# Kernel tuning notes

Hardware: AMD Instinct MI355X
Metric: run time of the kernel (lower is better)

The kernel has to match this reference:

```python
import jax, jax.numpy as jnp
import numpy as np

B, L, F, H, DIM = 32, 1024, 1024, 1024, 1024


def setup_inputs() -> dict:
    key = jax.random.key(0)
    ks = jax.random.split(key, 8)
    features = jax.random.normal(ks[0], (B, L, F), dtype=jnp.float32)
    hidden = jax.random.normal(ks[1], (B, H), dtype=jnp.float32)
    # Dense layer params (glorot-ish scale)
    W1 = jax.random.normal(ks[2], (F, DIM), dtype=jnp.float32) / np.sqrt(F)
    b1 = jnp.zeros((DIM,), dtype=jnp.float32)
    W2 = jax.random.normal(ks[3], (H, DIM), dtype=jnp.float32) / np.sqrt(H)
    b2 = jnp.zeros((DIM,), dtype=jnp.float32)
    Wp = jax.random.normal(ks[4], (DIM, 1), dtype=jnp.float32) / np.sqrt(DIM)
    bp = jnp.zeros((1,), dtype=jnp.float32)
    return {"features": features, "hidden": hidden, "W1": W1, "b1": b1,
            "W2": W2, "b2": b2, "Wp": Wp, "bp": bp}


def reference(features, hidden, W1, b1, W2, b2, Wp, bp):
    # features: [B, L, F], hidden: [B, H]
    h1 = jnp.einsum('blf,fd->bld', features, W1) + b1          # [B, L, D]
    h2 = (hidden @ W2 + b2)[:, None, :]                         # [B, 1, D]
    att = jnp.tanh(h1 + h2)                                     # [B, L, D]
    score = jnp.einsum('bld,do->blo', att, Wp) + bp             # [B, L, 1]
    attention_weights = jax.nn.softmax(score, axis=1)           # [B, L, 1]
    context_vector = jnp.sum(attention_weights * features, axis=1)  # [B, F]
    return context_vector
```

## Files before the change

kernel.cpp:

```cpp
#include <hip/hip_runtime.h>
#include <hip/hip_bf16.h>


typedef __attribute__((ext_vector_type(8))) __bf16 bf16x8;
typedef __attribute__((ext_vector_type(4))) float f32x4;

static __device__ __forceinline__ ushort f2bf(float x) {
  unsigned u = __float_as_uint(x);
  return (ushort)((u + 0x7fffu + ((u >> 16) & 1u)) >> 16);
}

static __device__ __forceinline__ int2 cvt4(float4 v) {
  __hip_bfloat162 c0 = __float22bfloat162_rn({v.x, v.y});
  __hip_bfloat162 c1 = __float22bfloat162_rn({v.z, v.w});
  int2 r;
  r.x = *(int*)&c0;
  r.y = *(int*)&c1;
  return r;
}

static __device__ __forceinline__ float tanh_fast(float x) {
  float e = __expf(2.f * x);
  return 1.f - 2.f / (e + 1.f);
}

__global__ __launch_bounds__(256) void prep_kernel(
    const float* __restrict__ W1, ushort* __restrict__ w1t,
    const float* __restrict__ hidden, const float* __restrict__ W2,
    const float* __restrict__ b2, float* __restrict__ h2p) {
  __shared__ float smem[64 * 65];
  const int bx = blockIdx.x, tid = threadIdx.x;
  if (bx < 256) {
    const int tc = bx & 15, tr = bx >> 4;
    float (*tt)[65] = (float(*)[65])smem;
    const int r = tid >> 4, c4 = (tid & 15) * 4;
#pragma unroll
    for (int p = 0; p < 4; ++p) {
      const int rr = p * 16 + r;
      float4 v = *(const float4*)(W1 + (size_t)(tr * 64 + rr) * 1024 + tc * 64 + c4);
      tt[rr][c4] = v.x; tt[rr][c4 + 1] = v.y; tt[rr][c4 + 2] = v.z; tt[rr][c4 + 3] = v.w;
    }
    __syncthreads();
    const int cc = tid >> 3, r8 = (tid & 7) * 8;
#pragma unroll
    for (int p = 0; p < 2; ++p) {
      const int c = p * 32 + cc;
      ushort tmp[8];
#pragma unroll
      for (int j = 0; j < 8; ++j) tmp[j] = f2bf(tt[r8 + j][c]);
      *(int4*)(w1t + (size_t)(tc * 64 + c) * 1024 + tr * 64 + r8) = *(int4*)tmp;
    }
  } else {
    const int t = bx - 256;
    const int dblk = t & 3, b = (t >> 2) & 31, z = t >> 7;
    const int d = dblk * 256 + tid;
    const int k0 = z * 128;
    float* h = smem;
    if (tid < 128) h[tid] = hidden[b * 1024 + k0 + tid];
    __syncthreads();
    float acc = (z == 0) ? b2[d] : 0.f;
#pragma unroll 8
    for (int k = 0; k < 128; ++k)
      acc += h[k] * W2[(size_t)(k0 + k) * 1024 + d];
    h2p[z * 32768 + b * 1024 + d] = acc;
  }
}


__global__ __launch_bounds__(512, 2) void gemm_score_kernel(
    const float* __restrict__ feat,
    const ushort* __restrict__ w1t,
    const float* __restrict__ b1, const float* __restrict__ h2p,
    const float* __restrict__ wp, float* __restrict__ score) {
  __shared__ ushort ldsA[2][64][32];
  __shared__ float hbl[1024], wpl[1024];
  __shared__ float sred[7][64];

  const int tid = threadIdx.x;
  const int row0 = blockIdx.x * 64;
  const int b = blockIdx.x >> 4;
  const int wave = tid >> 6, lane = tid & 63;
  const int lrow = lane & 15, quad = lane >> 4;

  {
    const int d = tid * 2;
    float2 hv = *(const float2*)(b1 + d);
#pragma unroll
    for (int p = 0; p < 8; ++p) {
      float2 hp = *(const float2*)(h2p + p * 32768 + b * 1024 + d);
      hv.x += hp.x;
      hv.y += hp.y;
    }
    *(float2*)(hbl + d) = hv;
    *(float2*)(wpl + d) = *(const float2*)(wp + d);
  }

  const int ar = tid >> 3;
  const int asw = ((((tid & 7) >> 1) ^ ((ar >> 1) & 3)) * 8 + (tid & 1) * 4);
  const float* aptr = feat + (size_t)(row0 + ar) * 1024 + (tid & 7) * 4;

  const int acs = (quad ^ ((lrow >> 1) & 3)) * 8;

  const ushort* bb[8];
#pragma unroll
  for (int j = 0; j < 8; ++j)
    bb[j] = w1t + (size_t)(wave * 128 + j * 16 + lrow) * 1024 + quad * 8;

  f32x4 acc[4][8] = {};
  float4 avv[2];
  bf16x8 bB[2][8];

  {
    float4 v0 = *(const float4*)(aptr);
    *(int2*)&ldsA[0][ar][asw] = cvt4(v0);
    avv[1] = *(const float4*)(aptr + 32);
    avv[0] = *(const float4*)(aptr + 64);
#pragma unroll
    for (int j = 0; j < 8; ++j) bB[0][j] = *(const bf16x8*)(bb[j]);
  }
  asm volatile("s_waitcnt lgkmcnt(0)");
  __builtin_amdgcn_sched_barrier(0);
  __builtin_amdgcn_s_barrier();
  __builtin_amdgcn_sched_barrier(0);

#pragma unroll
  for (int t = 0; t < 32; ++t) {
    const int cur = t & 1, nxt = cur ^ 1;
    bf16x8 af[4];
#pragma unroll
    for (int i = 0; i < 4; ++i)
      af[i] = *(const bf16x8*)&ldsA[cur][i * 16 + lrow][acs];
    if (t + 1 < 32) {
#pragma unroll
      for (int j = 0; j < 8; ++j)
        bB[nxt][j] = *(const bf16x8*)(bb[j] + (t + 1) * 32);
    }
    if (t + 1 < 32)
      *(int2*)&ldsA[nxt][ar][asw] = cvt4(avv[(t + 1) & 1]);
    if (t + 3 < 32)
      avv[(t + 1) & 1] = *(const float4*)(aptr + (t + 3) * 32);
    __builtin_amdgcn_s_setprio(1);
#pragma unroll
    for (int i = 0; i < 4; ++i)
#pragma unroll
      for (int j = 0; j < 8; ++j)
        acc[i][j] = __builtin_amdgcn_mfma_f32_16x16x32_bf16(
            af[i], bB[cur][j], acc[i][j], 0, 0, 0);
    __builtin_amdgcn_s_setprio(0);
    __builtin_amdgcn_sched_barrier(0);
    asm volatile("s_waitcnt lgkmcnt(0)");
    __builtin_amdgcn_sched_barrier(0);
    __builtin_amdgcn_s_barrier();
    __builtin_amdgcn_sched_barrier(0);
  }

  float hbv[8], wpv[8];
#pragma unroll
  for (int j = 0; j < 8; ++j) {
    const int c = wave * 128 + j * 16 + lrow;
    hbv[j] = hbl[c];
    wpv[j] = wpl[c];
  }
  float rsum[4][4];
#pragma unroll
  for (int i = 0; i < 4; ++i) {
#pragma unroll
    for (int r = 0; r < 4; ++r) {
      float s = 0.f;
#pragma unroll
      for (int j = 0; j < 8; ++j)
        s += tanh_fast(acc[i][j][r] + hbv[j]) * wpv[j];
      s += __shfl_xor(s, 8);
      s += __shfl_xor(s, 4);
      s += __shfl_xor(s, 2);
      s += __shfl_xor(s, 1);
      rsum[i][r] = s;
    }
  }
  if (wave != 0 && lrow == 0) {
#pragma unroll
    for (int i = 0; i < 4; ++i)
#pragma unroll
      for (int r = 0; r < 4; ++r)
        sred[wave - 1][i * 16 + quad * 4 + r] = rsum[i][r];
  }
  __syncthreads();
  if (wave == 0 && lrow == 0) {
#pragma unroll
    for (int i = 0; i < 4; ++i)
#pragma unroll
      for (int r = 0; r < 4; ++r) {
        const int ro = i * 16 + quad * 4 + r;
        float s = rsum[i][r];
#pragma unroll
        for (int w = 0; w < 7; ++w) s += sred[w][ro];
        score[row0 + ro] = s;
      }
  }
}

__global__ __launch_bounds__(256) void softmax_kernel(
    const float* __restrict__ score, float* __restrict__ w,
    float* __restrict__ out) {
  const int b = blockIdx.x, tid = threadIdx.x;
  const int lane = tid & 63, wv = tid >> 6;
  __shared__ float sm[4], ss[4];
  float v[4];
  float mx = -1e30f;
#pragma unroll
  for (int i = 0; i < 4; ++i) {
    const int idx = b * 1024 + i * 256 + tid;
    out[idx] = 0.f;
    v[i] = score[idx];
    mx = fmaxf(mx, v[i]);
  }
#pragma unroll
  for (int off = 32; off; off >>= 1) mx = fmaxf(mx, __shfl_xor(mx, off));
  if (lane == 0) sm[wv] = mx;
  __syncthreads();
  mx = fmaxf(fmaxf(sm[0], sm[1]), fmaxf(sm[2], sm[3]));
  float sum = 0.f;
#pragma unroll
  for (int i = 0; i < 4; ++i) {
    v[i] = __expf(v[i] - mx);
    sum += v[i];
  }
#pragma unroll
  for (int off = 32; off; off >>= 1) sum += __shfl_xor(sum, off);
  if (lane == 0) ss[wv] = sum;
  __syncthreads();
  const float inv = 1.f / (ss[0] + ss[1] + ss[2] + ss[3]);
#pragma unroll
  for (int i = 0; i < 4; ++i) w[b * 1024 + i * 256 + tid] = v[i] * inv;
}

__global__ __launch_bounds__(256) void context_kernel(
    const float* __restrict__ w, const float* __restrict__ feat,
    float* __restrict__ out) {
  const int b = blockIdx.y;
  const int l0 = blockIdx.x * 64;
  const int f0 = threadIdx.x * 4;
  __shared__ float wl[64];
  if (threadIdx.x < 64) wl[threadIdx.x] = w[b * 1024 + l0 + threadIdx.x];
  __syncthreads();
  const float* fb = feat + (size_t)b * 1048576 + (size_t)l0 * 1024 + f0;
  float a0 = 0.f, a1 = 0.f, a2 = 0.f, a3 = 0.f;
#pragma unroll 8
  for (int l = 0; l < 64; ++l) {
    float4 v = *(const float4*)(fb + (size_t)l * 1024);
    const float wv = wl[l];
    a0 += wv * v.x;
    a1 += wv * v.y;
    a2 += wv * v.z;
    a3 += wv * v.w;
  }
  float* dst = out + b * 1024 + f0;
  atomicAdd(dst + 0, a0);
  atomicAdd(dst + 1, a1);
  atomicAdd(dst + 2, a2);
  atomicAdd(dst + 3, a3);
}

extern "C" void kernel_launch(void* const* d_in, const int* in_sizes, int n_in,
                              void* d_out, int out_size, void* d_ws, size_t ws_size,
                              hipStream_t stream) {
  const float* feat   = (const float*)d_in[0];
  const float* hidden = (const float*)d_in[1];
  const float* W1     = (const float*)d_in[2];
  const float* b1     = (const float*)d_in[3];
  const float* W2     = (const float*)d_in[4];
  const float* b2     = (const float*)d_in[5];
  const float* Wp     = (const float*)d_in[6];
  float* out = (float*)d_out;

  char* ws = (char*)d_ws;
  ushort* w1t   = (ushort*)ws;
  float* score  = (float*)(ws + 2097152);
  float* h2p    = (float*)(ws + 3145728);
  float* wts    = (float*)(ws + 4194304);

  prep_kernel<<<1280, 256, 0, stream>>>(W1, w1t, hidden, W2, b2, h2p);
  gemm_score_kernel<<<512, 512, 0, stream>>>(feat, w1t, b1, h2p, Wp, score);
  softmax_kernel<<<32, 256, 0, stream>>>(score, wts, out);
  context_kernel<<<dim3(16, 32), 256, 0, stream>>>(wts, feat, out);
}
```

Before: 358.7 us.

## Retile score GEMM to 128x256 blocks with LDS-staged W1 and partial scores

Changes the GEMM from 64-row blocks that each cover the full 1024 output columns to 128x256 tiles on a 2D grid. W1 tiles are now loaded straight into LDS with global_load_lds instead of into per-wave registers. Because each block now covers only a quarter of the columns, it writes a partial score, and the softmax kernel sums the four partials. The aim is to cut redundant per-wave B traffic and raise arithmetic intensity. In exchange, each feature row is read by four column blocks, and there is an extra partial-score buffer plus a reduction step.

```diff
diff --git a/kernel.cpp b/kernel.cpp
--- a/kernel.cpp
+++ b/kernel.cpp
@@ -8,6 +8,12 @@
 static __device__ __forceinline__ ushort f2bf(float x) {
   unsigned u = __float_as_uint(x);
   return (ushort)((u + 0x7fffu + ((u >> 16) & 1u)) >> 16);
+}
+
+typedef __attribute__((address_space(1))) void gbl_t;
+typedef __attribute__((address_space(3))) void lds_t;
+static __device__ __forceinline__ void gl_lds16(const void* g, void* l) {
+  __builtin_amdgcn_global_load_lds((gbl_t*)g, (lds_t*)l, 16, 0, 0);
 }
 
 static __device__ __forceinline__ int2 cvt4(float4 v) {
@@ -67,140 +73,160 @@
 }
 
 
-__global__ __launch_bounds__(512, 2) void gemm_score_kernel(
+#define STAGE_B(T, BUF) {                                                      \
+    const int ko_ = (T) * 32;                                                  \
+    gl_lds16(w1t + b_go + ko_,          (char*)ldsB + (BUF) * 16384 + lB);     \
+    gl_lds16(w1t + b_go + 65536 + ko_,  (char*)ldsB + (BUF) * 16384 + lB + 4096); \
+    gl_lds16(w1t + b_go + 131072 + ko_, (char*)ldsB + (BUF) * 16384 + lB + 8192); \
+    gl_lds16(w1t + b_go + 196608 + ko_, (char*)ldsB + (BUF) * 16384 + lB + 12288); }
+
+__global__ __launch_bounds__(256, 2) void gemm_score_kernel(
     const float* __restrict__ feat,
     const ushort* __restrict__ w1t,
     const float* __restrict__ b1, const float* __restrict__ h2p,
-    const float* __restrict__ wp, float* __restrict__ score) {
-  __shared__ ushort ldsA[2][64][32];
-  __shared__ float hbl[1024], wpl[1024];
-  __shared__ float sred[7][64];
+    const float* __restrict__ wp, float* __restrict__ score_p) {
+  __shared__ ushort ldsA[2][128][32];
+  __shared__ ushort ldsB[2][256][32];
+  __shared__ float hbl[256], wpl[256];
+  __shared__ float sred[3][128];
 
   const int tid = threadIdx.x;
-  const int row0 = blockIdx.x * 64;
-  const int b = blockIdx.x >> 4;
+  const int col0 = blockIdx.x * 256;
+  const int row0 = blockIdx.y * 128;
+  const int b = blockIdx.y >> 3;
   const int wave = tid >> 6, lane = tid & 63;
   const int lrow = lane & 15, quad = lane >> 4;
+  const int acs = (quad ^ ((lrow >> 1) & 3)) * 8;
 
   {
-    const int d = tid * 2;
-    float2 hv = *(const float2*)(b1 + d);
-#pragma unroll
-    for (int p = 0; p < 8; ++p) {
-      float2 hp = *(const float2*)(h2p + p * 32768 + b * 1024 + d);
-      hv.x += hp.x;
-      hv.y += hp.y;
-    }
-    *(float2*)(hbl + d) = hv;
-    *(float2*)(wpl + d) = *(const float2*)(wp + d);
-  }
-
-  const int ar = tid >> 3;
-  const int asw = ((((tid & 7) >> 1) ^ ((ar >> 1) & 3)) * 8 + (tid & 1) * 4);
-  const float* aptr = feat + (size_t)(row0 + ar) * 1024 + (tid & 7) * 4;
-
-  const int acs = (quad ^ ((lrow >> 1) & 3)) * 8;
-
-  const ushort* bb[8];
-#pragma unroll
-  for (int j = 0; j < 8; ++j)
-    bb[j] = w1t + (size_t)(wave * 128 + j * 16 + lrow) * 1024 + quad * 8;
-
-  f32x4 acc[4][8] = {};
-  float4 avv[2];
-  bf16x8 bB[2][8];
-
+    const int d = col0 + tid;
+    float hv = b1[d];
+#pragma unroll
+    for (int p = 0; p < 8; ++p) hv += h2p[p * 32768 + b * 1024 + d];
+    hbl[tid] = hv;
+    wpl[tid] = wp[d];
+  }
+
+  int b_go, lB;
   {
-    float4 v0 = *(const float4*)(aptr);
-    *(int2*)&ldsA[0][ar][asw] = cvt4(v0);
-    avv[1] = *(const float4*)(aptr + 32);
-    avv[0] = *(const float4*)(aptr + 64);
-#pragma unroll
-    for (int j = 0; j < 8; ++j) bB[0][j] = *(const bf16x8*)(bb[j]);
-  }
-  asm volatile("s_waitcnt lgkmcnt(0)");
+    const int s = wave * 64 + lane;
+    const int r = s >> 2, c = s & 3;
+    const int q = c ^ ((r >> 1) & 3);
+    b_go = (col0 + r) * 1024 + q * 8;
+    lB = (wave * 64) * 16;
+  }
+
+  const int arow = tid >> 3;
+  const int akq = (tid & 7) >> 1;
+  const int xr = (arow >> 1) & 3;
+  const int awz = ((akq ^ xr) * 8) + (tid & 1) * 4;
+  const float* aptrA = feat + (size_t)(row0 + arow) * 1024 + (tid & 7) * 4;
+
+  f32x4 acc[8][4] = {};
+  float4 avv[2][4];
+
+  STAGE_B(0, 0);
+  __builtin_amdgcn_sched_barrier(0);
+#pragma unroll
+  for (int p = 0; p < 4; ++p) {
+    float4 v = *(const float4*)(aptrA + (size_t)p * 32768);
+    *(int2*)&ldsA[0][arow + 32 * p][awz] = cvt4(v);
+  }
+#pragma unroll
+  for (int p = 0; p < 4; ++p)
+    avv[1][p] = *(const float4*)(aptrA + (size_t)p * 32768 + 32);
+#pragma unroll
+  for (int p = 0; p < 4; ++p)
+    avv[0][p] = *(const float4*)(aptrA + (size_t)p * 32768 + 64);
+  asm volatile("s_waitcnt vmcnt(8) lgkmcnt(0)");
   __builtin_amdgcn_sched_barrier(0);
   __builtin_amdgcn_s_barrier();
-  __builtin_amdgcn_sched_barrier(0);
 
 #pragma unroll
   for (int t = 0; t < 32; ++t) {
     const int cur = t & 1, nxt = cur ^ 1;
-    bf16x8 af[4];
-#pragma unroll
-    for (int i = 0; i < 4; ++i)
-      af[i] = *(const bf16x8*)&ldsA[cur][i * 16 + lrow][acs];
+    if (t + 1 < 32) STAGE_B(t + 1, nxt);
+    __builtin_amdgcn_sched_barrier(0);
+    bf16x8 bfr0 = *(const bf16x8*)&ldsB[cur][wave * 64 + lrow][acs];
+    bf16x8 bfr1 = *(const bf16x8*)&ldsB[cur][wave * 64 + 16 + lrow][acs];
+    bf16x8 bfr2 = *(const bf16x8*)&ldsB[cur][wave * 64 + 32 + lrow][acs];
+    bf16x8 bfr3 = *(const bf16x8*)&ldsB[cur][wave * 64 + 48 + lrow][acs];
     if (t + 1 < 32) {
 #pragma unroll
-      for (int j = 0; j < 8; ++j)
-        bB[nxt][j] = *(const bf16x8*)(bb[j] + (t + 1) * 32);
-    }
-    if (t + 1 < 32)
-      *(int2*)&ldsA[nxt][ar][asw] = cvt4(avv[(t + 1) & 1]);
-    if (t + 3 < 32)
-      avv[(t + 1) & 1] = *(const float4*)(aptr + (t + 3) * 32);
+      for (int p = 0; p < 4; ++p)
+        *(int2*)&ldsA[nxt][arow + 32 * p][awz] = cvt4(avv[(t + 1) & 1][p]);
+    }
+    if (t + 3 < 32) {
+#pragma unroll
+      for (int p = 0; p < 4; ++p)
+        avv[(t + 1) & 1][p] =
+            *(const float4*)(aptrA + (size_t)p * 32768 + (t + 3) * 32);
+    }
     __builtin_amdgcn_s_setprio(1);
 #pragma unroll
-    for (int i = 0; i < 4; ++i)
-#pragma unroll
-      for (int j = 0; j < 8; ++j)
-        acc[i][j] = __builtin_amdgcn_mfma_f32_16x16x32_bf16(
-            af[i], bB[cur][j], acc[i][j], 0, 0, 0);
+    for (int i = 0; i < 8; ++i) {
+      const bf16x8 af = *(const bf16x8*)&ldsA[cur][i * 16 + lrow][acs];
+      acc[i][0] = __builtin_amdgcn_mfma_f32_16x16x32_bf16(af, bfr0, acc[i][0], 0, 0, 0);
+      acc[i][1] = __builtin_amdgcn_mfma_f32_16x16x32_bf16(af, bfr1, acc[i][1], 0, 0, 0);
+      acc[i][2] = __builtin_amdgcn_mfma_f32_16x16x32_bf16(af, bfr2, acc[i][2], 0, 0, 0);
+      acc[i][3] = __builtin_amdgcn_mfma_f32_16x16x32_bf16(af, bfr3, acc[i][3], 0, 0, 0);
+    }
     __builtin_amdgcn_s_setprio(0);
     __builtin_amdgcn_sched_barrier(0);
-    asm volatile("s_waitcnt lgkmcnt(0)");
+    if (t + 3 < 32) {
+      asm volatile("s_waitcnt vmcnt(4) lgkmcnt(0)");
+    } else {
+      asm volatile("s_waitcnt vmcnt(0) lgkmcnt(0)");
+    }
     __builtin_amdgcn_sched_barrier(0);
     __builtin_amdgcn_s_barrier();
-    __builtin_amdgcn_sched_barrier(0);
-  }
-
-  float hbv[8], wpv[8];
-#pragma unroll
-  for (int j = 0; j < 8; ++j) {
-    const int c = wave * 128 + j * 16 + lrow;
-    hbv[j] = hbl[c];
-    wpv[j] = wpl[c];
-  }
-  float rsum[4][4];
-#pragma unroll
-  for (int i = 0; i < 4; ++i) {
+  }
+
+  float hbv[4], wpv[4];
+#pragma unroll
+  for (int j = 0; j < 4; ++j) {
+    const int idx = wave * 64 + j * 16 + lrow;
+    hbv[j] = hbl[idx];
+    wpv[j] = wpl[idx];
+  }
+  float rs[8][4];
+#pragma unroll
+  for (int i = 0; i < 8; ++i) {
 #pragma unroll
     for (int r = 0; r < 4; ++r) {
       float s = 0.f;
 #pragma unroll
-      for (int j = 0; j < 8; ++j)
+      for (int j = 0; j < 4; ++j)
         s += tanh_fast(acc[i][j][r] + hbv[j]) * wpv[j];
       s += __shfl_xor(s, 8);
       s += __shfl_xor(s, 4);
       s += __shfl_xor(s, 2);
       s += __shfl_xor(s, 1);
-      rsum[i][r] = s;
+      rs[i][r] = s;
     }
   }
   if (wave != 0 && lrow == 0) {
 #pragma unroll
-    for (int i = 0; i < 4; ++i)
+    for (int i = 0; i < 8; ++i)
 #pragma unroll
       for (int r = 0; r < 4; ++r)
-        sred[wave - 1][i * 16 + quad * 4 + r] = rsum[i][r];
+        sred[wave - 1][i * 16 + quad * 4 + r] = rs[i][r];
   }
   __syncthreads();
   if (wave == 0 && lrow == 0) {
 #pragma unroll
-    for (int i = 0; i < 4; ++i)
+    for (int i = 0; i < 8; ++i)
 #pragma unroll
       for (int r = 0; r < 4; ++r) {
         const int ro = i * 16 + quad * 4 + r;
-        float s = rsum[i][r];
-#pragma unroll
-        for (int w = 0; w < 7; ++w) s += sred[w][ro];
-        score[row0 + ro] = s;
+        score_p[(size_t)blockIdx.x * 32768 + row0 + ro] =
+            rs[i][r] + sred[0][ro] + sred[1][ro] + sred[2][ro];
       }
   }
 }
 
 __global__ __launch_bounds__(256) void softmax_kernel(
-    const float* __restrict__ score, float* __restrict__ w,
+    const float* __restrict__ score_p, float* __restrict__ w,
     float* __restrict__ out) {
   const int b = blockIdx.x, tid = threadIdx.x;
   const int lane = tid & 63, wv = tid >> 6;
@@ -211,8 +237,11 @@
   for (int i = 0; i < 4; ++i) {
     const int idx = b * 1024 + i * 256 + tid;
     out[idx] = 0.f;
-    v[i] = score[idx];
-    mx = fmaxf(mx, v[i]);
+    float s = 0.f;
+#pragma unroll
+    for (int p = 0; p < 4; ++p) s += score_p[p * 32768 + idx];
+    v[i] = s;
+    mx = fmaxf(mx, s);
   }
 #pragma unroll
   for (int off = 32; off; off >>= 1) mx = fmaxf(mx, __shfl_xor(mx, off));
@@ -274,13 +303,14 @@
   float* out = (float*)d_out;
 
   char* ws = (char*)d_ws;
-  ushort* w1t   = (ushort*)ws;
-  float* score  = (float*)(ws + 2097152);
-  float* h2p    = (float*)(ws + 3145728);
-  float* wts    = (float*)(ws + 4194304);
+  ushort* w1t    = (ushort*)ws;
+  float* score_p = (float*)(ws + 2097152);
+  float* h2p     = (float*)(ws + 3145728);
+  float* wts     = (float*)(ws + 4194304);
 
   prep_kernel<<<1280, 256, 0, stream>>>(W1, w1t, hidden, W2, b2, h2p);
-  gemm_score_kernel<<<512, 512, 0, stream>>>(feat, w1t, b1, h2p, Wp, score);
-  softmax_kernel<<<32, 256, 0, stream>>>(score, wts, out);
+  gemm_score_kernel<<<dim3(4, 256), 256, 0, stream>>>(feat, w1t, b1, h2p, Wp,
+                                                      score_p);
+  softmax_kernel<<<32, 256, 0, stream>>>(score_p, wts, out);
   context_kernel<<<dim3(16, 32), 256, 0, stream>>>(wts, feat, out);
 }
```

After: 324.3 us. 9.6% less time.
